# Performance work log

Hardware: AMD Instinct MI355X
Metric: run time of the kernel (lower is better)

## Reference

```python
import jax, jax.numpy as jnp
import numpy as np
from jax import lax

D_MODEL = 1024
N_GROUPS = 8
SUB_SIZE = 8192
TOP_K = 32
BATCH = 2048


def setup_inputs() -> dict:
    key = jax.random.key(0)
    kx, ke, kb, kd = jax.random.split(key, 4)
    x = jax.random.normal(kx, (BATCH, D_MODEL), dtype=jnp.float32)
    # encoder weights: torch Linear(d_model, size) -> W_enc[g]: [d_model, size]
    W_enc = jax.random.normal(ke, (N_GROUPS, D_MODEL, SUB_SIZE), dtype=jnp.float32) * (1.0 / np.sqrt(D_MODEL))
    b_enc = jax.random.normal(kb, (N_GROUPS, SUB_SIZE), dtype=jnp.float32) * 0.01
    # decoder weights: torch Linear(size, d_model, bias=False).weight is [d_model, size];
    # init normalizes over dim=0 (d_model). We store W_dec[g]: [size, d_model] (= weight.T),
    # so normalize over the last axis.
    W_dec = jax.random.normal(kd, (N_GROUPS, SUB_SIZE, D_MODEL), dtype=jnp.float32)
    W_dec = W_dec / (jnp.linalg.norm(W_dec, axis=-1, keepdims=True) + 1e-8)
    return {"x": x, "W_enc": W_enc, "b_enc": b_enc, "W_dec": W_dec}


def reference(x, W_enc, b_enc, W_dec):
    G, B, S = N_GROUPS, x.shape[0], SUB_SIZE
    # per-group encode: [G, B, S]
    pre = jnp.einsum('bd,gds->gbs', x, W_enc) + b_enc[:, None, :]
    # top-k mask per group (same k for all groups -> batched lax.top_k)
    _, idxs = lax.top_k(pre, TOP_K)  # idxs: [G, B, k]
    gi = jnp.arange(G)[:, None, None]
    bi = jnp.arange(B)[None, :, None]
    mask = jnp.zeros_like(pre).at[gi, bi, idxs].set(1.0)
    acts = jax.nn.relu(pre) * mask  # [G, B, S]
    # per-group decode, summed across groups: [B, d_model]
    final_recon = jnp.einsum('gbs,gsd->bd', acts, W_dec)
    # concatenation of per-group acts along feature dim: [B, G*S]
    full_acts = jnp.transpose(acts, (1, 0, 2)).reshape(B, G * S)
    return (final_recon, full_acts)
```

## Files before the change

### kernel.cpp

```cpp
#include <hip/hip_runtime.h>

#define D_MODEL 1024
#define NGROUPS 8
#define SUB 8192
#define TOPK 32
#define BATCH 2048
#define NTOT (NGROUPS * SUB)

typedef float v4f __attribute__((ext_vector_type(4)));
typedef _Float16 f16x8 __attribute__((ext_vector_type(8)));
typedef _Float16 f16x4 __attribute__((ext_vector_type(4)));
typedef float f32x4 __attribute__((ext_vector_type(4)));

__device__ __forceinline__ unsigned fkey(float f) {
    unsigned u = __float_as_uint(f);
    return (u & 0x80000000u) ? ~u : (u | 0x80000000u);
}
__device__ __forceinline__ float inv_fkey(unsigned key) {
    unsigned u = (key & 0x80000000u) ? (key & 0x7FFFFFFFu) : ~key;
    return __uint_as_float(u);
}

__global__ __launch_bounds__(256) void cvt_x_h(
    const float* __restrict__ x, _Float16* __restrict__ xh)
{
    const size_t i = ((size_t)blockIdx.x * 256 + threadIdx.x) * 8;
    const v4f a = *(const v4f*)(x + i);
    const v4f b = *(const v4f*)(x + i + 4);
    f16x8 h;
#pragma unroll
    for (int j = 0; j < 4; ++j) { h[j] = (_Float16)a[j]; h[4 + j] = (_Float16)b[j]; }
    *(f16x8*)(xh + i) = h;
}

__global__ __launch_bounds__(256) void cvt_wdec_h(
    const float* __restrict__ Wd, _Float16* __restrict__ Wh)
{
    const size_t i = ((size_t)blockIdx.x * 256 + threadIdx.x) * 8;
    const v4f a = *(const v4f*)(Wd + i);
    const v4f b = *(const v4f*)(Wd + i + 4);
    f16x8 h;
#pragma unroll
    for (int j = 0; j < 4; ++j) { h[j] = (_Float16)a[j]; h[4 + j] = (_Float16)b[j]; }
    *(f16x8*)(Wh + i) = h;
}

__global__ __launch_bounds__(256) void prezero_acts(float* __restrict__ out_acts)
{
    float4* p4 = (float4*)out_acts;
    const int tid = threadIdx.x;
#pragma unroll
    for (int i = 0; i < 8; ++i) {
        const size_t flat = (size_t)blockIdx.x * 2048 + (size_t)i * 256 + tid;
        const size_t r = flat >> 10, o = flat & 1023;
        p4[r * 2048 + 1024 + o] = make_float4(0.f, 0.f, 0.f, 0.f);
    }
}

__global__ __launch_bounds__(256) void transpose_wenc2(
    const float* __restrict__ W, float* __restrict__ WT, _Float16* __restrict__ WhT)
{
    __shared__ float t[32][33];
    const int g = blockIdx.z, kt = blockIdx.y, st = blockIdx.x;
    const int lx = threadIdx.x & 31, ly = threadIdx.x >> 5;
    const float* Wg = W + (size_t)g * D_MODEL * SUB;
    float* WTg = WT + (size_t)g * SUB * D_MODEL;
    _Float16* WhTg = WhT + (size_t)g * SUB * D_MODEL;
#pragma unroll
    for (int r = 0; r < 4; ++r)
        t[ly + 8 * r][lx] = Wg[(size_t)(kt * 32 + ly + 8 * r) * SUB + st * 32 + lx];
    __syncthreads();
#pragma unroll
    for (int r = 0; r < 4; ++r) {
        const float v = t[lx][ly + 8 * r];
        const size_t o = (size_t)(st * 32 + ly + 8 * r) * D_MODEL + kt * 32 + lx;
        WTg[o] = v;
        WhTg[o] = (_Float16)v;
    }
}

__global__ __launch_bounds__(256) void mfma_scores_u(
    const _Float16* __restrict__ xh, const _Float16* __restrict__ WhT,
    const float* __restrict__ b_enc, _Float16* __restrict__ sb, const int scale)
{
    __shared__ _Float16 Ah[128 * 40];
    __shared__ _Float16 Bh[128 * 40];

    const int tid = threadIdx.x;
    const int wblk = blockIdx.x;
    const int t = (wblk & 7) * 1024 + (wblk >> 3);
    const int mt = t & 15, nt = t >> 4;
    const int g = nt >> 6;
    const int sbase = (nt & 63) * 128;
    const int mbase = mt * 128;

    const int lane = tid & 63, w = tid >> 6;
    const int wm = w >> 1, wn = w & 1;
    const int l15 = lane & 15, grp = lane >> 4;

    const int sr = tid >> 1, kh16 = (tid & 1) * 16;

    const _Float16* Agp = xh + (size_t)mbase * D_MODEL;
    const _Float16* Bgp = WhT + ((size_t)g * SUB + sbase) * D_MODEL;

    f32x4 acc[4][4];
#pragma unroll
    for (int i = 0; i < 4; ++i)
#pragma unroll
        for (int j = 0; j < 4; ++j) acc[i][j] = (f32x4){0.f, 0.f, 0.f, 0.f};

#pragma unroll 1
    for (int it = 0; it < 32; ++it) {
        const int k0 = it * 32;
        const f16x8 a0 = *(const f16x8*)(Agp + (size_t)sr * D_MODEL + k0 + kh16);
        const f16x8 a1 = *(const f16x8*)(Agp + (size_t)sr * D_MODEL + k0 + kh16 + 8);
        const f16x8 b0 = *(const f16x8*)(Bgp + (size_t)sr * D_MODEL + k0 + kh16);
        const f16x8 b1 = *(const f16x8*)(Bgp + (size_t)sr * D_MODEL + k0 + kh16 + 8);

        *(f16x8*)&Ah[sr * 40 + kh16]     = a0;
        *(f16x8*)&Ah[sr * 40 + kh16 + 8] = a1;
        *(f16x8*)&Bh[sr * 40 + kh16]     = b0;
        *(f16x8*)&Bh[sr * 40 + kh16 + 8] = b1;
        __syncthreads();

        f16x8 af[4], bf[4];
#pragma unroll
        for (int i = 0; i < 4; ++i)
            af[i] = *(const f16x8*)&Ah[(wm * 64 + i * 16 + l15) * 40 + 8 * grp];
#pragma unroll
        for (int j = 0; j < 4; ++j)
            bf[j] = *(const f16x8*)&Bh[(wn * 64 + j * 16 + l15) * 40 + 8 * grp];
#pragma unroll
        for (int i = 0; i < 4; ++i)
#pragma unroll
            for (int j = 0; j < 4; ++j)
                acc[i][j] = __builtin_amdgcn_mfma_f32_16x16x32_f16(af[i], bf[j], acc[i][j], 0, 0, 0);
        __syncthreads();
    }

    float bb[4];
#pragma unroll
    for (int j = 0; j < 4; ++j)
        bb[j] = b_enc[(size_t)g * SUB + sbase + wn * 64 + j * 16 + l15];
#pragma unroll
    for (int i = 0; i < 4; ++i) {
        const int row = mbase + wm * 64 + i * 16 + grp * 4;
#pragma unroll
        for (int j = 0; j < 4; ++j) {
            const int cols = sbase + wn * 64 + j * 16 + l15;
#pragma unroll
            for (int r = 0; r < 4; ++r) {
                _Float16* hg = sb + ((size_t)(row + r) * NTOT + (size_t)g * SUB) * (size_t)scale;
                hg[cols] = (_Float16)__fadd_rn(acc[i][j][r], bb[j]);
            }
        }
    }
}

#define CCAP 128
#define BCAP 512

__global__ __launch_bounds__(256) void select_decode_u(
    const float* __restrict__ x, const float* __restrict__ WT,
    const float* __restrict__ b_enc, const _Float16* __restrict__ Wd_h,
    float* __restrict__ out_recon, float* __restrict__ out_acts,
    const _Float16* __restrict__ sb, const int scale, const int do_zero)
{
    __shared__ float xrow[1024];
    __shared__ unsigned hist[256], sscan[256], wsum[4];
    __shared__ unsigned sh_bin, sh_above, cert_cnt, band_cnt;
    __shared__ int   cert_idx[CCAP];
    __shared__ float cert_val[CCAP];
    __shared__ int   band_idx[BCAP];
    __shared__ float band_val[BCAP];
    __shared__ int   gcend[4], gbend[4];
    __shared__ int   sel_idx[TOPK];
    __shared__ float sel_val[TOPK];

    const int tid = threadIdx.x;
    const int lane = tid & 63;
    const int w = tid >> 6;
    const size_t b = blockIdx.x >> 1;
    const int h = blockIdx.x & 1;
    const int g0 = h * 4;

    *(float4*)&xrow[tid * 4] = *(const float4*)(x + b * D_MODEL + tid * 4);
    if (tid == 0) { cert_cnt = 0; band_cnt = 0; }
    float r0 = 0.f, r1 = 0.f, r2 = 0.f, r3 = 0.f;

    for (int gi = 0; gi < 4; ++gi) {
        const int g = g0 + gi;
        const _Float16* hg = sb + (b * NTOT + (size_t)g * SUB) * (size_t)scale;
        float sc[32];
#pragma unroll
        for (int t = 0; t < 4; ++t) {
            const f16x8 hv = *(const f16x8*)(hg + (size_t)(tid + t * 256) * 8);
#pragma unroll
            for (int e = 0; e < 8; ++e) sc[t * 8 + e] = (float)hv[e];
        }

        hist[tid] = 0;
        __syncthreads();
#pragma unroll
        for (int j = 0; j < 32; ++j)
            atomicAdd(&hist[fkey(sc[j]) >> 24], 1u);
        __syncthreads();

        unsigned prefix = 0, kwant = TOPK;
#pragma unroll
        for (int r = 0; r < 2; ++r) {
            unsigned s = hist[tid];
#pragma unroll
            for (int off = 1; off < 64; off <<= 1) {
                const unsigned o = __shfl_down(s, off, 64);
                if (lane + off < 64) s += o;
            }
            if (lane == 0) wsum[w] = s;
            __syncthreads();
            unsigned add = 0;
            for (int w2 = w + 1; w2 < 4; ++w2) add += wsum[w2];
            s += add;
            sscan[tid] = s;
            __syncthreads();
            const unsigned snext = (tid < 255) ? sscan[tid + 1] : 0u;
            if (s >= kwant && snext < kwant) { sh_bin = (unsigned)tid; sh_above = snext; }
            __syncthreads();
            const int shift = 24 - 8 * r;
            prefix |= sh_bin << shift;
            kwant -= sh_above;
            __syncthreads();
            if (r == 0) {
                hist[tid] = 0;
                __syncthreads();
#pragma unroll
                for (int j = 0; j < 32; ++j) {
                    const unsigned key = fkey(sc[j]);
                    if ((key >> 24) == (prefix >> 24))
                        atomicAdd(&hist[(key >> 16) & 255u], 1u);
                }
                __syncthreads();
            }
        }
        const float F = inv_fkey(prefix);
        const unsigned supkey = fkey(F - 0.06f);
        const unsigned inkey  = fkey(F + 0.077f);

#pragma unroll
        for (int j = 0; j < 32; ++j) {
            const unsigned key = fkey(sc[j]);
            if (key >= supkey) {
                const int sidx = (tid + (j >> 3) * 256) * 8 + (j & 7);
                if (key > inkey) {
                    const unsigned slot = atomicAdd(&cert_cnt, 1u);
                    if (slot < CCAP) { cert_idx[slot] = (g << 13) | sidx; cert_val[slot] = fmaxf(sc[j], 0.f); }
                } else {
                    const unsigned slot = atomicAdd(&band_cnt, 1u);
                    if (slot < BCAP) band_idx[slot] = (g << 13) | sidx;
                }
            }
        }
        __syncthreads();
        if (tid == 0) { gcend[gi] = (int)min(cert_cnt, (unsigned)CCAP);
                        gbend[gi] = (int)min(band_cnt, (unsigned)BCAP); }
        __syncthreads();
    }

    if (do_zero) {
        for (int gi = 0; gi < 4; ++gi) {
            float* rz = out_acts + b * NTOT + (size_t)(g0 + gi) * SUB;
#pragma unroll
            for (int t = 0; t < 4; ++t)
                *(float4*)(rz + (size_t)(tid + t * 256) * 4) = make_float4(0.f, 0.f, 0.f, 0.f);
        }
        __syncthreads();
    }

    const int bcnt = gbend[3];
    for (int base = 0; base < bcnt; base += 256) {
        const int c = base + tid;
        if (c < bcnt) {
            const int id = band_idx[c];
            const int g = id >> 13, sidx = id & 8191;
            const float* col = WT + ((size_t)g * SUB + sidx) * D_MODEL;
            float a0 = 0.f, a1 = 0.f, a2 = 0.f;
#pragma unroll 4
            for (int q = 0; q < 64; ++q) {
                const float4 w0 = *(const float4*)(col + q * 4);
                const float4 w1 = *(const float4*)(col + 384 + q * 4);
                const float4 w2 = *(const float4*)(col + 768 + q * 4);
                a0 = fmaf(xrow[q * 4 + 0], w0.x, a0); a1 = fmaf(xrow[384 + q * 4 + 0], w1.x, a1); a2 = fmaf(xrow[768 + q * 4 + 0], w2.x, a2);
                a0 = fmaf(xrow[q * 4 + 1], w0.y, a0); a1 = fmaf(xrow[384 + q * 4 + 1], w1.y, a1); a2 = fmaf(xrow[768 + q * 4 + 1], w2.y, a2);
                a0 = fmaf(xrow[q * 4 + 2], w0.z, a0); a1 = fmaf(xrow[384 + q * 4 + 2], w1.z, a1); a2 = fmaf(xrow[768 + q * 4 + 2], w2.z, a2);
                a0 = fmaf(xrow[q * 4 + 3], w0.w, a0); a1 = fmaf(xrow[384 + q * 4 + 3], w1.w, a1); a2 = fmaf(xrow[768 + q * 4 + 3], w2.w, a2);
            }
#pragma unroll 4
            for (int q = 64; q < 96; ++q) {
                const float4 w0 = *(const float4*)(col + q * 4);
                const float4 w1 = *(const float4*)(col + 384 + q * 4);
                a0 = fmaf(xrow[q * 4 + 0], w0.x, a0); a1 = fmaf(xrow[384 + q * 4 + 0], w1.x, a1);
                a0 = fmaf(xrow[q * 4 + 1], w0.y, a0); a1 = fmaf(xrow[384 + q * 4 + 1], w1.y, a1);
                a0 = fmaf(xrow[q * 4 + 2], w0.z, a0); a1 = fmaf(xrow[384 + q * 4 + 2], w1.z, a1);
                a0 = fmaf(xrow[q * 4 + 3], w0.w, a0); a1 = fmaf(xrow[384 + q * 4 + 3], w1.w, a1);
            }
            band_val[c] = __fadd_rn(__fadd_rn(__fadd_rn(a0, a1), a2),
                                    b_enc[(size_t)g * SUB + sidx]);
        }
    }
    __syncthreads();

    for (int gi = 0; gi < 4; ++gi) {
        const int g = g0 + gi;
        const int cb = (gi == 0) ? 0 : gcend[gi - 1];
        const int ce = gcend[gi];
        const int n_in = ce - cb;
        const int n_slots = TOPK - n_in;
        const int bb = (gi == 0) ? 0 : gbend[gi - 1];
        const int be = gbend[gi];

        if (tid < n_in) { sel_idx[tid] = cert_idx[cb + tid] & 8191; sel_val[tid] = cert_val[cb + tid]; }
        for (int t = bb + tid; t < be; t += 256) {
            const unsigned mykey = fkey(band_val[t]);
            const int mys = band_idx[t] & 8191;
            int rank = 0;
            for (int e = bb; e < be; ++e) {
                const unsigned ke = fkey(band_val[e]);
                if (ke > mykey || (ke == mykey && (band_idx[e] & 8191) < mys)) ++rank;
            }
            if (rank < n_slots) { sel_idx[n_in + rank] = mys; sel_val[n_in + rank] = fmaxf(band_val[t], 0.f); }
        }
        __syncthreads();

        float* rowg = out_acts + b * NTOT + (size_t)g * SUB;
        if (tid < TOPK) rowg[sel_idx[tid]] = sel_val[tid];

        const _Float16* Wgh = Wd_h + (size_t)g * SUB * D_MODEL + tid * 4;
#pragma unroll 8
        for (int j = 0; j < TOPK; ++j) {
            const float v = sel_val[j];
            const f16x4 wv = *(const f16x4*)(Wgh + (size_t)sel_idx[j] * D_MODEL);
            r0 = fmaf(v, (float)wv[0], r0); r1 = fmaf(v, (float)wv[1], r1);
            r2 = fmaf(v, (float)wv[2], r2); r3 = fmaf(v, (float)wv[3], r3);
        }
        __syncthreads();
    }
    float* rp = out_recon + b * D_MODEL + tid * 4;
    atomicAdd(rp + 0, r0); atomicAdd(rp + 1, r1);
    atomicAdd(rp + 2, r2); atomicAdd(rp + 3, r3);
}

#define PIDX(s) ((s) + ((s) >> 5))
#define BM 64
#define BN 128
#define BK 16
#define LDSA 68
#define LDSB 132

__global__ __launch_bounds__(256) void fb_encode_gemm(
    const float* __restrict__ x, const float* __restrict__ W_enc,
    const float* __restrict__ b_enc, float* __restrict__ out_acts)
{
    __shared__ float As[BK * LDSA];
    __shared__ float Bs[BK * LDSB];
    const int tid = threadIdx.x;
    const int nt = blockIdx.x, mt = blockIdx.y;
    const int g = nt >> 6, sbase = (nt & 63) * BN, mbase = mt * BM;
    const float* Bp = W_enc + ((size_t)g * D_MODEL) * SUB + sbase;
    const float* Ap = x + (size_t)mbase * D_MODEL;
    const int a_m = tid >> 2, a_c = (tid & 3) * 4;
    const int b_k = tid >> 5, b_c = (tid & 31) * 4;
    const int tr = tid >> 4, tc = tid & 15;
    float tot[4][8], cur[4][8];
#pragma unroll
    for (int i = 0; i < 4; ++i)
#pragma unroll
        for (int j = 0; j < 8; ++j) { tot[i][j] = 0.f; cur[i][j] = 0.f; }
#pragma unroll 1
    for (int it = 0; it < 64; ++it) {
        const int k0 = it * BK;
        const v4f va = *(const v4f*)(Ap + (size_t)a_m * D_MODEL + k0 + a_c);
        const v4f vb0 = *(const v4f*)(Bp + (size_t)(k0 + b_k) * SUB + b_c);
        const v4f vb1 = *(const v4f*)(Bp + (size_t)(k0 + b_k + 8) * SUB + b_c);
#pragma unroll
        for (int j = 0; j < 4; ++j) As[(a_c + j) * LDSA + a_m] = va[j];
        *(v4f*)&Bs[b_k * LDSB + b_c] = vb0;
        *(v4f*)&Bs[(b_k + 8) * LDSB + b_c] = vb1;
        __syncthreads();
        if (it == 24 || it == 48) {
#pragma unroll
            for (int i = 0; i < 4; ++i)
#pragma unroll
                for (int j = 0; j < 8; ++j) { tot[i][j] = __fadd_rn(tot[i][j], cur[i][j]); cur[i][j] = 0.f; }
        }
#pragma unroll
        for (int kk = 0; kk < BK; ++kk) {
            float a[4], bb[8];
            *(v4f*)&a[0] = *(const v4f*)&As[kk * LDSA + tr * 4];
            *(v4f*)&bb[0] = *(const v4f*)&Bs[kk * LDSB + tc * 4];
            *(v4f*)&bb[4] = *(const v4f*)&Bs[kk * LDSB + tc * 4 + 64];
#pragma unroll
            for (int i = 0; i < 4; ++i)
#pragma unroll
                for (int j = 0; j < 8; ++j) cur[i][j] = fmaf(a[i], bb[j], cur[i][j]);
        }
        __syncthreads();
    }
#pragma unroll
    for (int i = 0; i < 4; ++i)
#pragma unroll
        for (int j = 0; j < 8; ++j) tot[i][j] = __fadd_rn(tot[i][j], cur[i][j]);
    const float* bias = b_enc + (size_t)g * SUB + sbase;
    const float4 bb0 = *(const float4*)(bias + tc * 4);
    const float4 bb1 = *(const float4*)(bias + tc * 4 + 64);
    float* outp = out_acts + (size_t)g * SUB + sbase;
#pragma unroll
    for (int i = 0; i < 4; ++i) {
        const size_t row = (size_t)(mbase + tr * 4 + i);
        const float4 o0 = make_float4(__fadd_rn(tot[i][0], bb0.x), __fadd_rn(tot[i][1], bb0.y),
                                      __fadd_rn(tot[i][2], bb0.z), __fadd_rn(tot[i][3], bb0.w));
        const float4 o1 = make_float4(__fadd_rn(tot[i][4], bb1.x), __fadd_rn(tot[i][5], bb1.y),
                                      __fadd_rn(tot[i][6], bb1.z), __fadd_rn(tot[i][7], bb1.w));
        *(float4*)(outp + row * NTOT + tc * 4) = o0;
        *(float4*)(outp + row * NTOT + tc * 4 + 64) = o1;
    }
}

__global__ __launch_bounds__(256) void fb_topk_decode(
    const float* __restrict__ W_dec, float* __restrict__ out_recon,
    float* __restrict__ out_acts)
{
    __shared__ float row[SUB + (SUB >> 5)];
    __shared__ unsigned hist[256], sscan[256], wsum[4], wsum2[4];
    __shared__ unsigned sh_bin, sh_above;
    __shared__ int sel_idx[TOPK];
    __shared__ float sel_val[TOPK];
    const int tid = threadIdx.x, lane = tid & 63, w = tid >> 6;
    const size_t b = blockIdx.x;
    float r0 = 0.f, r1 = 0.f, r2 = 0.f, r3 = 0.f;
    for (int g = 0; g < NGROUPS; ++g) {
        float* rowg = out_acts + b * NTOT + (size_t)g * SUB;
#pragma unroll
        for (int t = 0; t < 8; ++t) {
            const int i4 = tid + t * 256;
            const float4 v = *(const float4*)(rowg + (size_t)i4 * 4);
            const int s0 = i4 * 4;
            row[PIDX(s0) + 0] = v.x; row[PIDX(s0) + 1] = v.y;
            row[PIDX(s0) + 2] = v.z; row[PIDX(s0) + 3] = v.w;
        }
        __syncthreads();
        unsigned prefix = 0, kwant = TOPK;
#pragma unroll
        for (int r = 0; r < 4; ++r) {
            const int shift = 24 - 8 * r;
            hist[tid] = 0;
            __syncthreads();
            for (int j = 0; j < 32; ++j) {
                const unsigned key = fkey(row[tid * 33 + j]);
                const unsigned hi = (unsigned)(((unsigned long long)key) >> (shift + 8));
                const unsigned pi = (unsigned)(((unsigned long long)prefix) >> (shift + 8));
                if (hi == pi) atomicAdd(&hist[(key >> shift) & 255u], 1u);
            }
            __syncthreads();
            unsigned s = hist[tid];
#pragma unroll
            for (int off = 1; off < 64; off <<= 1) {
                const unsigned o = __shfl_down(s, off, 64);
                if (lane + off < 64) s += o;
            }
            if (lane == 0) wsum[w] = s;
            __syncthreads();
            unsigned add = 0;
            for (int w2 = w + 1; w2 < 4; ++w2) add += wsum[w2];
            s += add;
            sscan[tid] = s;
            __syncthreads();
            const unsigned snext = (tid < 255) ? sscan[tid + 1] : 0u;
            if (s >= kwant && snext < kwant) { sh_bin = (unsigned)tid; sh_above = snext; }
            __syncthreads();
            prefix |= sh_bin << shift;
            kwant -= sh_above;
            __syncthreads();
        }
        const unsigned T = prefix, n_take = kwant, cnt_gt_total = TOPK - n_take;
        unsigned loc_gt = 0, loc_eq = 0;
        for (int j = 0; j < 32; ++j) {
            const unsigned key = fkey(row[tid * 33 + j]);
            loc_gt += (key > T); loc_eq += (key == T);
        }
        const unsigned pack = loc_gt | (loc_eq << 16);
        unsigned sI = pack;
#pragma unroll
        for (int off = 1; off < 64; off <<= 1) {
            const unsigned o = __shfl_up(sI, off, 64);
            if (lane >= off) sI += o;
        }
        if (lane == 63) wsum2[w] = sI;
        __syncthreads();
        unsigned woff = 0;
        for (int w2 = 0; w2 < w; ++w2) woff += wsum2[w2];
        const unsigned excl = sI - pack + woff;
        unsigned run_gt = excl & 0xFFFFu, run_eq = excl >> 16;
        for (int j = 0; j < 32; ++j) {
            const int sidx = tid * 32 + j;
            const float f = row[tid * 33 + j];
            const unsigned key = fkey(f);
            const float act = fmaxf(f, 0.f);
            if (key > T) { sel_idx[run_gt] = sidx; sel_val[run_gt] = act; ++run_gt; row[tid * 33 + j] = act; }
            else if (key == T) {
                if (run_eq < n_take) { sel_idx[cnt_gt_total + run_eq] = sidx; sel_val[cnt_gt_total + run_eq] = act; row[tid * 33 + j] = act; }
                else row[tid * 33 + j] = 0.f;
                ++run_eq;
            } else row[tid * 33 + j] = 0.f;
        }
        __syncthreads();
#pragma unroll
        for (int t = 0; t < 8; ++t) {
            const int i4 = tid + t * 256;
            const int s0 = i4 * 4;
            *(float4*)(rowg + (size_t)i4 * 4) =
                make_float4(row[PIDX(s0)], row[PIDX(s0) + 1], row[PIDX(s0) + 2], row[PIDX(s0) + 3]);
        }
        const float* Wg = W_dec + (size_t)g * SUB * D_MODEL + tid * 4;
#pragma unroll 8
        for (int j = 0; j < TOPK; ++j) {
            const float v = sel_val[j];
            const float4 wv = *(const float4*)(Wg + (size_t)sel_idx[j] * D_MODEL);
            r0 = fmaf(v, wv.x, r0); r1 = fmaf(v, wv.y, r1);
            r2 = fmaf(v, wv.z, r2); r3 = fmaf(v, wv.w, r3);
        }
        __syncthreads();
    }
    *(float4*)(out_recon + b * D_MODEL + tid * 4) = make_float4(r0, r1, r2, r3);
}

extern "C" void kernel_launch(void* const* d_in, const int* in_sizes, int n_in,
                              void* d_out, int out_size, void* d_ws, size_t ws_size,
                              hipStream_t stream) {
    const float* x     = (const float*)d_in[0];
    const float* W_enc = (const float*)d_in[1];
    const float* b_enc = (const float*)d_in[2];
    const float* W_dec = (const float*)d_in[3];

    float* out_recon = (float*)d_out;
    float* out_acts  = (float*)d_out + (size_t)BATCH * D_MODEL;

    const size_t WT_BYTES = (size_t)NGROUPS * SUB * D_MODEL * 4;
    const size_t WH_BYTES = (size_t)NGROUPS * SUB * D_MODEL * 2;
    const size_t WD_BYTES = (size_t)NGROUPS * SUB * D_MODEL * 2;
    const size_t XH_BYTES = (size_t)BATCH * D_MODEL * 2;
    const size_t SC_BYTES = (size_t)BATCH * NTOT * 2;

    if (ws_size >= WT_BYTES + WH_BYTES + WD_BYTES + XH_BYTES + SC_BYTES) {
        float* WT = (float*)d_ws;
        _Float16* WhT = (_Float16*)((char*)d_ws + WT_BYTES);
        _Float16* WdH = (_Float16*)((char*)d_ws + WT_BYTES + WH_BYTES);
        _Float16* xh  = (_Float16*)((char*)d_ws + WT_BYTES + WH_BYTES + WD_BYTES);
        _Float16* SC  = (_Float16*)((char*)d_ws + WT_BYTES + WH_BYTES + WD_BYTES + XH_BYTES);
        hipMemsetAsync(out_recon, 0, (size_t)BATCH * D_MODEL * 4, stream);
        hipMemsetAsync(out_acts, 0, (size_t)BATCH * NTOT * 4, stream);
        cvt_x_h<<<BATCH * D_MODEL / 2048, 256, 0, stream>>>(x, xh);
        cvt_wdec_h<<<NGROUPS * SUB * D_MODEL / 2048, 256, 0, stream>>>(W_dec, WdH);
        transpose_wenc2<<<dim3(SUB / 32, D_MODEL / 32, NGROUPS), 256, 0, stream>>>(W_enc, WT, WhT);
        mfma_scores_u<<<8192, 256, 0, stream>>>(xh, WhT, b_enc, SC, 1);
        select_decode_u<<<BATCH * 2, 256, 0, stream>>>(x, WT, b_enc, WdH, out_recon, out_acts, SC, 1, 0);
    } else if (ws_size >= WT_BYTES + WH_BYTES + WD_BYTES + XH_BYTES) {
        float* WT = (float*)d_ws;
        _Float16* WhT = (_Float16*)((char*)d_ws + WT_BYTES);
        _Float16* WdH = (_Float16*)((char*)d_ws + WT_BYTES + WH_BYTES);
        _Float16* xh  = (_Float16*)((char*)d_ws + WT_BYTES + WH_BYTES + WD_BYTES);
        hipMemsetAsync(out_recon, 0, (size_t)BATCH * D_MODEL * 4, stream);
        cvt_x_h<<<BATCH * D_MODEL / 2048, 256, 0, stream>>>(x, xh);
        cvt_wdec_h<<<NGROUPS * SUB * D_MODEL / 2048, 256, 0, stream>>>(W_dec, WdH);
        transpose_wenc2<<<dim3(SUB / 32, D_MODEL / 32, NGROUPS), 256, 0, stream>>>(W_enc, WT, WhT);
        prezero_acts<<<8192, 256, 0, stream>>>(out_acts);
        mfma_scores_u<<<8192, 256, 0, stream>>>(xh, WhT, b_enc, (_Float16*)out_acts, 2);
        select_decode_u<<<BATCH * 2, 256, 0, stream>>>(x, WT, b_enc, WdH, out_recon, out_acts,
                                                      (const _Float16*)out_acts, 2, 1);
    } else {
        fb_encode_gemm<<<dim3(NTOT / BN, BATCH / BM), 256, 0, stream>>>(x, W_enc, b_enc, out_acts);
        fb_topk_decode<<<BATCH, 256, 0, stream>>>(W_dec, out_recon, out_acts);
    }
}
```

Before: 1.265 ms.

## Load MFMA fragments directly from global memory, dropping LDS staging

The score GEMM no longer stages A and B tiles through shared memory with two barriers per k-step. Each wave now reads its MFMA fragments straight from global memory and relies on L2/L1 to serve the reuse across waves. The launcher also drops the separate-workspace score buffer path, so scores always go into the output acts buffer. In exchange, global/L2 traffic rises about twofold, because each operand row is read by two waves, and the per-lane 16-byte row-strided loads are less coalesced.

```diff
diff --git a/kernel.cpp b/kernel.cpp
--- a/kernel.cpp
+++ b/kernel.cpp
@@ -79,13 +79,10 @@
     }
 }
 
-__global__ __launch_bounds__(256) void mfma_scores_u(
+__global__ __launch_bounds__(256) void mfma_scores_l2(
     const _Float16* __restrict__ xh, const _Float16* __restrict__ WhT,
     const float* __restrict__ b_enc, _Float16* __restrict__ sb, const int scale)
 {
-    __shared__ _Float16 Ah[128 * 40];
-    __shared__ _Float16 Bh[128 * 40];
-
     const int tid = threadIdx.x;
     const int wblk = blockIdx.x;
     const int t = (wblk & 7) * 1024 + (wblk >> 3);
@@ -98,10 +95,14 @@
     const int wm = w >> 1, wn = w & 1;
     const int l15 = lane & 15, grp = lane >> 4;
 
-    const int sr = tid >> 1, kh16 = (tid & 1) * 16;
-
-    const _Float16* Agp = xh + (size_t)mbase * D_MODEL;
-    const _Float16* Bgp = WhT + ((size_t)g * SUB + sbase) * D_MODEL;
+    const _Float16* Ab[4];
+    const _Float16* Bb[4];
+#pragma unroll
+    for (int i = 0; i < 4; ++i)
+        Ab[i] = xh + (size_t)(mbase + wm * 64 + i * 16 + l15) * D_MODEL + 8 * grp;
+#pragma unroll
+    for (int j = 0; j < 4; ++j)
+        Bb[j] = WhT + ((size_t)g * SUB + sbase + wn * 64 + j * 16 + l15) * D_MODEL + 8 * grp;
 
     f32x4 acc[4][4];
 #pragma unroll
@@ -112,30 +113,16 @@
 #pragma unroll 1
     for (int it = 0; it < 32; ++it) {
         const int k0 = it * 32;
-        const f16x8 a0 = *(const f16x8*)(Agp + (size_t)sr * D_MODEL + k0 + kh16);
-        const f16x8 a1 = *(const f16x8*)(Agp + (size_t)sr * D_MODEL + k0 + kh16 + 8);
-        const f16x8 b0 = *(const f16x8*)(Bgp + (size_t)sr * D_MODEL + k0 + kh16);
-        const f16x8 b1 = *(const f16x8*)(Bgp + (size_t)sr * D_MODEL + k0 + kh16 + 8);
-
-        *(f16x8*)&Ah[sr * 40 + kh16]     = a0;
-        *(f16x8*)&Ah[sr * 40 + kh16 + 8] = a1;
-        *(f16x8*)&Bh[sr * 40 + kh16]     = b0;
-        *(f16x8*)&Bh[sr * 40 + kh16 + 8] = b1;
-        __syncthreads();
-
         f16x8 af[4], bf[4];
 #pragma unroll
-        for (int i = 0; i < 4; ++i)
-            af[i] = *(const f16x8*)&Ah[(wm * 64 + i * 16 + l15) * 40 + 8 * grp];
-#pragma unroll
-        for (int j = 0; j < 4; ++j)
-            bf[j] = *(const f16x8*)&Bh[(wn * 64 + j * 16 + l15) * 40 + 8 * grp];
+        for (int i = 0; i < 4; ++i) af[i] = *(const f16x8*)(Ab[i] + k0);
+#pragma unroll
+        for (int j = 0; j < 4; ++j) bf[j] = *(const f16x8*)(Bb[j] + k0);
 #pragma unroll
         for (int i = 0; i < 4; ++i)
 #pragma unroll
             for (int j = 0; j < 4; ++j)
                 acc[i][j] = __builtin_amdgcn_mfma_f32_16x16x32_f16(af[i], bf[j], acc[i][j], 0, 0, 0);
-        __syncthreads();
     }
 
     float bb[4];
@@ -547,22 +534,8 @@
     const size_t WH_BYTES = (size_t)NGROUPS * SUB * D_MODEL * 2;
     const size_t WD_BYTES = (size_t)NGROUPS * SUB * D_MODEL * 2;
     const size_t XH_BYTES = (size_t)BATCH * D_MODEL * 2;
-    const size_t SC_BYTES = (size_t)BATCH * NTOT * 2;
-
-    if (ws_size >= WT_BYTES + WH_BYTES + WD_BYTES + XH_BYTES + SC_BYTES) {
-        float* WT = (float*)d_ws;
-        _Float16* WhT = (_Float16*)((char*)d_ws + WT_BYTES);
-        _Float16* WdH = (_Float16*)((char*)d_ws + WT_BYTES + WH_BYTES);
-        _Float16* xh  = (_Float16*)((char*)d_ws + WT_BYTES + WH_BYTES + WD_BYTES);
-        _Float16* SC  = (_Float16*)((char*)d_ws + WT_BYTES + WH_BYTES + WD_BYTES + XH_BYTES);
-        hipMemsetAsync(out_recon, 0, (size_t)BATCH * D_MODEL * 4, stream);
-        hipMemsetAsync(out_acts, 0, (size_t)BATCH * NTOT * 4, stream);
-        cvt_x_h<<<BATCH * D_MODEL / 2048, 256, 0, stream>>>(x, xh);
-        cvt_wdec_h<<<NGROUPS * SUB * D_MODEL / 2048, 256, 0, stream>>>(W_dec, WdH);
-        transpose_wenc2<<<dim3(SUB / 32, D_MODEL / 32, NGROUPS), 256, 0, stream>>>(W_enc, WT, WhT);
-        mfma_scores_u<<<8192, 256, 0, stream>>>(xh, WhT, b_enc, SC, 1);
-        select_decode_u<<<BATCH * 2, 256, 0, stream>>>(x, WT, b_enc, WdH, out_recon, out_acts, SC, 1, 0);
-    } else if (ws_size >= WT_BYTES + WH_BYTES + WD_BYTES + XH_BYTES) {
+
+    if (ws_size >= WT_BYTES + WH_BYTES + WD_BYTES + XH_BYTES) {
         float* WT = (float*)d_ws;
         _Float16* WhT = (_Float16*)((char*)d_ws + WT_BYTES);
         _Float16* WdH = (_Float16*)((char*)d_ws + WT_BYTES + WH_BYTES);
@@ -572,7 +545,7 @@
         cvt_wdec_h<<<NGROUPS * SUB * D_MODEL / 2048, 256, 0, stream>>>(W_dec, WdH);
         transpose_wenc2<<<dim3(SUB / 32, D_MODEL / 32, NGROUPS), 256, 0, stream>>>(W_enc, WT, WhT);
         prezero_acts<<<8192, 256, 0, stream>>>(out_acts);
-        mfma_scores_u<<<8192, 256, 0, stream>>>(xh, WhT, b_enc, (_Float16*)out_acts, 2);
+        mfma_scores_l2<<<8192, 256, 0, stream>>>(xh, WhT, b_enc, (_Float16*)out_acts, 2);
         select_decode_u<<<BATCH * 2, 256, 0, stream>>>(x, WT, b_enc, WdH, out_recon, out_acts,
                                                       (const _Float16*)out_acts, 2, 1);
     } else {
```

After: 1.750 ms. 1.38x slower.
